# Kernel optimization log

Measured on AMD Instinct MI355X. Metric: run time of the kernel, lower is better.

Reference implementation:

```python
import jax, jax.numpy as jnp
import numpy as np

# Dims (match init_kwargs)
B, S, D = 2, 2048, 2048
H = 16
Q_LORA, KV_LORA = 768, 512
NOPE, ROPE, VD = 128, 64, 128
QHD = NOPE + ROPE  # 192


def setup_inputs() -> dict:
    key = jax.random.key(0)
    ks = jax.random.split(key, 7)
    w = lambda k, shape: (jax.random.normal(k, shape, jnp.float32) * 0.02)
    return {
        "x": jax.random.normal(ks[0], (B, S, D), jnp.float32),
        "position": jnp.broadcast_to(jnp.arange(S, dtype=jnp.int32), (B, S)),
        "mask": jnp.tril(jnp.ones((1, 1, S, S), jnp.int32)),  # causal
        "w_q_down": w(ks[1], (D, Q_LORA)),                 # (in, out) layout
        "w_q_up": w(ks[2], (Q_LORA, H * QHD)),
        "w_kv_down": w(ks[3], (D, KV_LORA + ROPE)),
        "w_kv_up": w(ks[4], (KV_LORA, H * (NOPE + VD))),
        "w_out": w(ks[5], (H * VD, D)),
    }


def reference(x, position, mask, w_q_down, w_q_up, w_kv_down, w_kv_up, w_out):
    # position unused: rope_embedding is None in the source module.
    # Low-rank Q: down then up projection.
    q = (x @ w_q_down) @ w_q_up                      # [B,S,H*QHD]
    q = q.reshape(B, S, H, QHD).transpose(0, 2, 1, 3)  # [B,H,S,QHD]
    q_nope, q_rope = q[..., :NOPE], q[..., NOPE:]

    # Low-rank KV: down projection yields compressed kv + shared rope key.
    c = x @ w_kv_down                                # [B,S,KV_LORA+ROPE]
    c_kv, k_rope = c[..., :KV_LORA], c[..., KV_LORA:]
    k_rope = k_rope[:, None, :, :]                   # [B,1,S,ROPE]

    kv = (c_kv @ w_kv_up).reshape(B, S, H, NOPE + VD).transpose(0, 2, 1, 3)
    k_nope, v = kv[..., :NOPE], kv[..., NOPE:]       # [B,H,S,NOPE], [B,H,S,VD]

    q_state = jnp.concatenate([q_nope, q_rope], axis=-1)           # [B,H,S,QHD]
    k_state = jnp.concatenate(
        [k_nope, jnp.broadcast_to(k_rope, (B, H, S, ROPE))], axis=-1)

    scale = 1.0 / jnp.sqrt(jnp.float32(VD))  # source divides by sqrt(v_head_dim)
    scores = jnp.einsum("bhqd,bhkd->bhqk", q_state, k_state) * scale
    scores = jnp.where(mask == 0, jnp.float32(-jnp.inf), scores)
    att = jax.nn.softmax(scores, axis=-1)            # dropout_rate=0 (eval)
    out = jnp.einsum("bhqk,bhkd->bhqd", att, v)      # [B,H,S,VD]
    out = out.transpose(0, 2, 1, 3).reshape(B, S, H * VD)
    return out @ w_out
```

## Files before the change

kernel.cpp:

```cpp
#include <hip/hip_runtime.h>

typedef __bf16 bf16;
typedef bf16 bf16x8 __attribute__((ext_vector_type(8)));
typedef bf16 bf16x4 __attribute__((ext_vector_type(4)));
typedef float f32x4 __attribute__((ext_vector_type(4)));
typedef short s16x4 __attribute__((ext_vector_type(4)));

#define AS1 __attribute__((address_space(1)))
#define AS3 __attribute__((address_space(3)))

__device__ __forceinline__ void load_lds16(const void* g, void* l) {
    __builtin_amdgcn_global_load_lds((const AS1 unsigned int*)g,
                                     (AS3 unsigned int*)l, 16, 0, 0);
}

__global__ __launch_bounds__(256) void cast_f32_bf16(
        const float* __restrict__ in, bf16* __restrict__ out, int n) {
    int i = (blockIdx.x * 256 + threadIdx.x) * 4;
    if (i < n) {
        float4 v = *(const float4*)(in + i);
        bf16x4 o = { (bf16)v.x, (bf16)v.y, (bf16)v.z, (bf16)v.w };
        *(bf16x4*)(out + i) = o;
    }
}

__global__ __launch_bounds__(256) void transpose_cast(
        const float* __restrict__ in, bf16* __restrict__ out,
        int K, int N, int Np) {
    __shared__ float tile[32][33];
    int bx = blockIdx.x * 32;
    int by = blockIdx.y * 32;
    int tx = threadIdx.x, ty = threadIdx.y;
#pragma unroll
    for (int i = 0; i < 4; ++i) {
        int k = by + ty + i * 8, n = bx + tx;
        float v = (k < K && n < N) ? in[(size_t)k * N + n] : 0.f;
        tile[ty + i * 8][tx] = v;
    }
    __syncthreads();
#pragma unroll
    for (int i = 0; i < 4; ++i) {
        int n = bx + ty + i * 8, k = by + tx;
        if (n < Np && k < K) out[(size_t)n * K + k] = (bf16)tile[tx][ty + i * 8];
    }
}

__global__ __launch_bounds__(256) void transpose_v(
        const bf16* __restrict__ kvb, bf16* __restrict__ vtb) {
    __shared__ bf16 t[32][34];
    const int kv0 = blockIdx.x * 32;
    const int vd0 = blockIdx.y * 32;
    const int bh = blockIdx.z;
    const int b = bh >> 4, h = bh & 15;
    const int tx = threadIdx.x, ty = threadIdx.y;
#pragma unroll
    for (int i = 0; i < 4; ++i)
        t[ty + i * 8][tx] = kvb[(size_t)(b * 2048 + kv0 + ty + i * 8) * 4096
                                + h * 256 + 128 + vd0 + tx];
    __syncthreads();
#pragma unroll
    for (int i = 0; i < 4; ++i)
        vtb[(size_t)(bh * 128 + vd0 + ty + i * 8) * 2048 + kv0 + tx] =
            t[tx][ty + i * 8];
}

template <typename OutT>
__global__ __launch_bounds__(256) void gemm_bt(
        const bf16* __restrict__ A, const bf16* __restrict__ Bt,
        OutT* __restrict__ C, int K, int lda, int ldb, int ldc) {
    __shared__ __align__(16) bf16 As[128 * 64];
    __shared__ __align__(16) bf16 Bs[128 * 64];
    const int tid = threadIdx.x;
    const int wave = tid >> 6, lane = tid & 63;
    const int l15 = lane & 15, quad = lane >> 4;
    const int m0 = blockIdx.y * 128, n0 = blockIdx.x * 128;
    const int wm = (wave >> 1) * 64, wn = (wave & 1) * 64;

    f32x4 acc[4][4] = {};

    for (int k0 = 0; k0 < K; k0 += 64) {
#pragma unroll
        for (int c = 0; c < 4; ++c) {
            int e = wave * 2048 + c * 512 + lane * 8;
            int r = e >> 6, col = e & 63;
            load_lds16(A + (size_t)(m0 + r) * lda + k0 + col,
                       &As[wave * 2048 + c * 512]);
            load_lds16(Bt + (size_t)(n0 + r) * ldb + k0 + col,
                       &Bs[wave * 2048 + c * 512]);
        }
        __syncthreads();
#pragma unroll
        for (int kk = 0; kk < 64; kk += 32) {
            bf16x8 af[4], bf[4];
#pragma unroll
            for (int i = 0; i < 4; ++i)
                af[i] = *(const bf16x8*)&As[(wm + i * 16 + l15) * 64 + kk + quad * 8];
#pragma unroll
            for (int j = 0; j < 4; ++j)
                bf[j] = *(const bf16x8*)&Bs[(wn + j * 16 + l15) * 64 + kk + quad * 8];
#pragma unroll
            for (int i = 0; i < 4; ++i)
#pragma unroll
                for (int j = 0; j < 4; ++j)
                    acc[i][j] = __builtin_amdgcn_mfma_f32_16x16x32_bf16(
                        af[i], bf[j], acc[i][j], 0, 0, 0);
        }
        __syncthreads();
    }
#pragma unroll
    for (int i = 0; i < 4; ++i)
#pragma unroll
        for (int j = 0; j < 4; ++j) {
            int row = m0 + wm + i * 16 + quad * 4;
            int col = n0 + wn + j * 16 + l15;
#pragma unroll
            for (int r = 0; r < 4; ++r)
                C[(size_t)(row + r) * ldc + col] = (OutT)acc[i][j][r];
        }
}

__global__ __launch_bounds__(256) void gemm_down(
        const bf16* __restrict__ A, const bf16* __restrict__ Bt,
        bf16* __restrict__ C1, bf16* __restrict__ C2) {
    const int K = 2048, lda = 2048, ldb = 2048;
    __shared__ __align__(16) bf16 As[128 * 64];
    __shared__ __align__(16) bf16 Bs[128 * 64];
    const int tid = threadIdx.x;
    const int wave = tid >> 6, lane = tid & 63;
    const int l15 = lane & 15, quad = lane >> 4;
    const int m0 = blockIdx.y * 128, n0 = blockIdx.x * 128;
    const int wm = (wave >> 1) * 64, wn = (wave & 1) * 64;

    f32x4 acc[4][4] = {};

    for (int k0 = 0; k0 < K; k0 += 64) {
#pragma unroll
        for (int c = 0; c < 4; ++c) {
            int e = wave * 2048 + c * 512 + lane * 8;
            int r = e >> 6, col = e & 63;
            load_lds16(A + (size_t)(m0 + r) * lda + k0 + col,
                       &As[wave * 2048 + c * 512]);
            load_lds16(Bt + (size_t)(n0 + r) * ldb + k0 + col,
                       &Bs[wave * 2048 + c * 512]);
        }
        __syncthreads();
#pragma unroll
        for (int kk = 0; kk < 64; kk += 32) {
            bf16x8 af[4], bf[4];
#pragma unroll
            for (int i = 0; i < 4; ++i)
                af[i] = *(const bf16x8*)&As[(wm + i * 16 + l15) * 64 + kk + quad * 8];
#pragma unroll
            for (int j = 0; j < 4; ++j)
                bf[j] = *(const bf16x8*)&Bs[(wn + j * 16 + l15) * 64 + kk + quad * 8];
#pragma unroll
            for (int i = 0; i < 4; ++i)
#pragma unroll
                for (int j = 0; j < 4; ++j)
                    acc[i][j] = __builtin_amdgcn_mfma_f32_16x16x32_bf16(
                        af[i], bf[j], acc[i][j], 0, 0, 0);
        }
        __syncthreads();
    }
    bf16* Cp; int ldc, coff;
    if (n0 < 768) { Cp = C1; ldc = 768; coff = 0; }
    else          { Cp = C2; ldc = 640; coff = 768; }
#pragma unroll
    for (int i = 0; i < 4; ++i)
#pragma unroll
        for (int j = 0; j < 4; ++j) {
            int row = m0 + wm + i * 16 + quad * 4;
            int col = n0 + wn + j * 16 + l15 - coff;
#pragma unroll
            for (int r = 0; r < 4; ++r)
                Cp[(size_t)(row + r) * ldc + col] = (bf16)acc[i][j][r];
        }
}

__global__ __launch_bounds__(1024, 4) void mla_attention_split(
        const bf16* __restrict__ qb, const bf16* __restrict__ kvb,
        const bf16* __restrict__ cb, const bf16* __restrict__ vtb,
        bf16* __restrict__ ob, bf16* __restrict__ part_o,
        float* __restrict__ part_ml) {
    constexpr int S = 2048;
    const signed char k_of[20]  = {7,7,7,7, 6,6,6,6, 5,5,5, 4,4,4, 3,3, 2,2, 1, 0};
    const signed char c_of[20]  = {0,1,2,3, 0,1,2,3, 0,1,2, 0,1,2, 0,1, 0,1, 0, 0};
    const signed char np_of[8]  = {1,1,2,2,3,3,4,4};
    const signed char pre_of[8] = {0,0,0,1,2,4,6,9};

    const int k  = k_of[blockIdx.x], c = c_of[blockIdx.x];
    const int np = np_of[k];
    const int h = blockIdx.y, b = blockIdx.z;
    const int T  = 4 * k + 4;
    const int t0 = (c * T) / np, t1 = ((c + 1) * T) / np;
    const int q0 = k * 256;

    const int tid = threadIdx.x, wave = tid >> 6, lane = tid & 63;
    const int l15 = lane & 15, quad = lane >> 4;

    __shared__ __align__(16) bf16 Ks[2][24 * 512];
    __shared__ __align__(16) bf16 Vs[2][8 * 1024];

    const int qrow = q0 + wave * 16 + l15;
    bf16x8 qf[6];
    {
        const bf16* qr = qb + (size_t)(b * S + qrow) * 3072 + h * 192;
#pragma unroll
        for (int ks = 0; ks < 6; ++ks)
            qf[ks] = *(const bf16x8*)(qr + ks * 32 + quad * 8);
    }

    const bf16* vt_head = vtb + (size_t)((b * 16 + h) * 128) * 2048;

    auto stage = [&](int kt, int bufi) {
        const int kv0 = kt * 64;
        if (wave < 8) {
            const int mt = wave >> 1;
            const size_t row = (size_t)(b * S + kv0 + mt * 16 + l15);
#pragma unroll
            for (int i = 0; i < 3; ++i) {
                const int ks = (wave & 1) * 3 + i;
                const bf16* g = (ks < 4)
                    ? kvb + row * 4096 + h * 256 + ks * 32 + quad * 8
                    : cb  + row * 640  + 512 + (ks - 4) * 32 + quad * 8;
                load_lds16(g, &Ks[bufi][(mt * 6 + ks) * 512]);
            }
        } else {
            const int nt = wave - 8;
#pragma unroll
            for (int i = 0; i < 2; ++i) {
                const bf16* g = vt_head + (size_t)(nt * 16 + l15) * 2048
                                + kv0 + (i * 4 + quad) * 8;
                load_lds16(g, &Vs[bufi][nt * 1024 + i * 512]);
            }
        }
    };

    f32x4 o[8] = {};
    float m_i = -1e30f, l_i = 0.f;
    const float sm_scale = 0.08838834764831845f * 1.4426950408889634f;
    const int qmin_w = q0 + wave * 16;

    stage(t0, 0);
    stage(t0 + 1, 1);

    int cur = 0;
    for (int kt = t0; kt < t1; ++kt, cur ^= 1) {
        const int kv0 = kt * 64;

        if (kt + 1 < t1) {
            if (wave < 8) asm volatile("s_waitcnt vmcnt(3)" ::: "memory");
            else          asm volatile("s_waitcnt vmcnt(2)" ::: "memory");
        } else {
            asm volatile("s_waitcnt vmcnt(0)" ::: "memory");
        }
        __builtin_amdgcn_s_barrier();
        __builtin_amdgcn_sched_barrier(0);

        f32x4 s[4];
        __builtin_amdgcn_s_setprio(1);
#pragma unroll
        for (int mt = 0; mt < 4; ++mt) {
            f32x4 a = {};
#pragma unroll
            for (int ks = 0; ks < 6; ++ks) {
                bf16x8 kf = *(const bf16x8*)&Ks[cur][(mt * 6 + ks) * 512 + lane * 8];
                a = __builtin_amdgcn_mfma_f32_16x16x32_bf16(kf, qf[ks], a, 0, 0, 0);
            }
            s[mt] = a;
        }
        __builtin_amdgcn_s_setprio(0);

        if (kv0 + 63 > qmin_w) {
#pragma unroll
            for (int mt = 0; mt < 4; ++mt)
#pragma unroll
                for (int r = 0; r < 4; ++r) {
                    int kvi = kv0 + mt * 16 + quad * 4 + r;
                    s[mt][r] = (kvi <= qrow) ? s[mt][r] * sm_scale : -1e30f;
                }
        } else {
#pragma unroll
            for (int mt = 0; mt < 4; ++mt)
#pragma unroll
                for (int r = 0; r < 4; ++r)
                    s[mt][r] = s[mt][r] * sm_scale;
        }
        float mx4[4];
#pragma unroll
        for (int mt = 0; mt < 4; ++mt)
            mx4[mt] = fmaxf(fmaxf(s[mt][0], s[mt][1]),
                            fmaxf(s[mt][2], s[mt][3]));
        float mx = fmaxf(fmaxf(mx4[0], mx4[1]), fmaxf(mx4[2], mx4[3]));
        mx = fmaxf(mx, __shfl_xor(mx, 16, 64));
        mx = fmaxf(mx, __shfl_xor(mx, 32, 64));
        float m_new = fmaxf(m_i, mx);
        float su4[4];
        bf16x4 pf[4];
#pragma unroll
        for (int mt = 0; mt < 4; ++mt) {
            float e0 = exp2f(s[mt][0] - m_new);
            float e1 = exp2f(s[mt][1] - m_new);
            float e2 = exp2f(s[mt][2] - m_new);
            float e3 = exp2f(s[mt][3] - m_new);
            su4[mt] = (e0 + e1) + (e2 + e3);
            pf[mt][0] = (bf16)e0; pf[mt][1] = (bf16)e1;
            pf[mt][2] = (bf16)e2; pf[mt][3] = (bf16)e3;
        }
        float su = (su4[0] + su4[1]) + (su4[2] + su4[3]);
        su += __shfl_xor(su, 16, 64);
        su += __shfl_xor(su, 32, 64);
        if (__all(mx <= m_i)) {
            l_i += su;
        } else {
            float alpha = exp2f(m_i - m_new);
            l_i = l_i * alpha + su;
            m_i = m_new;
            float alpha_r[4];
#pragma unroll
            for (int r = 0; r < 4; ++r)
                alpha_r[r] = __shfl(alpha, quad * 4 + r, 64);
#pragma unroll
            for (int nt = 0; nt < 8; ++nt)
#pragma unroll
                for (int r = 0; r < 4; ++r) o[nt][r] *= alpha_r[r];
        }

        __builtin_amdgcn_s_setprio(1);
#pragma unroll
        for (int ktk = 0; ktk < 4; ++ktk) {
            s16x4 a = __builtin_bit_cast(s16x4, pf[ktk]);
            const int voff = ktk * 256 + (quad >> 1) * 128 + l15 * 8 + (quad & 1) * 4;
#pragma unroll
            for (int nt = 0; nt < 8; ++nt) {
                s16x4 bfv = __builtin_bit_cast(s16x4,
                    *(const bf16x4*)&Vs[cur][nt * 1024 + voff]);
                o[nt] = __builtin_amdgcn_mfma_f32_16x16x16bf16_1k(a, bfv, o[nt], 0, 0, 0);
            }
        }
        __builtin_amdgcn_s_setprio(0);

        __builtin_amdgcn_s_barrier();
        if (kt + 2 < t1) stage(kt + 2, cur);
    }

    if (np == 1) {
        float l_r[4];
#pragma unroll
        for (int r = 0; r < 4; ++r) l_r[r] = __shfl(l_i, quad * 4 + r, 64);
        bf16* obase = ob + (size_t)(b * S + q0 + wave * 16) * 2048 + h * 128;
#pragma unroll
        for (int nt = 0; nt < 8; ++nt)
#pragma unroll
            for (int r = 0; r < 4; ++r)
                obase[(size_t)(quad * 4 + r) * 2048 + nt * 16 + l15] =
                    (bf16)(o[nt][r] / l_r[r]);
    } else {
        const int bh = b * 16 + h;
        if (quad == 0) {
            const int qlocal = wave * 16 + l15;
            float* mlp = part_ml + ((size_t)(bh * 8 + k) * 4 + c) * 512;
            mlp[qlocal] = m_i;
            mlp[256 + qlocal] = l_i;
        }
        if (c == np - 1) {
            bf16* obase = ob + (size_t)(b * S + q0 + wave * 16) * 2048 + h * 128;
#pragma unroll
            for (int nt = 0; nt < 8; ++nt)
#pragma unroll
                for (int r = 0; r < 4; ++r)
                    obase[(size_t)(quad * 4 + r) * 2048 + nt * 16 + l15] =
                        (bf16)o[nt][r];
        } else {
            bf16* pb = part_o + (size_t)(bh * 12 + pre_of[k] + c) * 32768
                       + (size_t)(wave * 16) * 128;
#pragma unroll
            for (int nt = 0; nt < 8; ++nt)
#pragma unroll
                for (int r = 0; r < 4; ++r)
                    pb[(quad * 4 + r) * 128 + nt * 16 + l15] = (bf16)o[nt][r];
        }
    }
}

__global__ __launch_bounds__(256) void mla_merge(
        const bf16* __restrict__ part_o, const float* __restrict__ part_ml,
        bf16* __restrict__ ob) {
    const signed char np_of[8]  = {1,1,2,2,3,3,4,4};
    const signed char pre_of[8] = {0,0,0,1,2,4,6,9};
    const int k = 2 + blockIdx.x;
    const int h = blockIdx.y, b = blockIdx.z;
    const int bh = b * 16 + h;
    const int np = np_of[k];
    const int row = threadIdx.x;

    const float* mlb = part_ml + (size_t)(bh * 8 + k) * 4 * 512;
    const float m0 = mlb[row],            l0 = mlb[256 + row];
    const float m1 = mlb[512 + row],      l1 = mlb[512 + 256 + row];
    const float m2 = (np > 2) ? mlb[1024 + row] : -1e30f;
    const float l2 = (np > 2) ? mlb[1024 + 256 + row] : 0.f;
    const float m3 = (np > 3) ? mlb[1536 + row] : -1e30f;
    const float l3 = (np > 3) ? mlb[1536 + 256 + row] : 0.f;
    const float M = fmaxf(fmaxf(m0, m1), fmaxf(m2, m3));
    float a0 = exp2f(m0 - M), a1 = exp2f(m1 - M);
    float a2 = exp2f(m2 - M), a3 = exp2f(m3 - M);
    const float inv = 1.f / (l0 * a0 + l1 * a1 + l2 * a2 + l3 * a3);
    a0 *= inv; a1 *= inv; a2 *= inv; a3 *= inv;
    const float alast = (np == 2) ? a1 : (np == 3) ? a2 : a3;

    const bf16* p0 = part_o + (size_t)(bh * 12 + pre_of[k]) * 32768 + row * 128;
    const bf16* p1 = p0 + 32768;
    const bf16* p2 = p1 + 32768;
    bf16* po = ob + (size_t)(b * 2048 + k * 256 + row) * 2048 + h * 128;
#pragma unroll
    for (int i = 0; i < 16; ++i) {
        bf16x8 vb = *(const bf16x8*)(po + i * 8);
        bf16x8 v0 = *(const bf16x8*)(p0 + i * 8);
        float acc[8];
#pragma unroll
        for (int u = 0; u < 8; ++u)
            acc[u] = (float)vb[u] * alast + (float)v0[u] * a0;
        if (np > 2) {
            bf16x8 v1 = *(const bf16x8*)(p1 + i * 8);
#pragma unroll
            for (int u = 0; u < 8; ++u) acc[u] += (float)v1[u] * a1;
        }
        if (np > 3) {
            bf16x8 v2 = *(const bf16x8*)(p2 + i * 8);
#pragma unroll
            for (int u = 0; u < 8; ++u) acc[u] += (float)v2[u] * a2;
        }
        bf16x8 om;
#pragma unroll
        for (int u = 0; u < 8; ++u) om[u] = (bf16)acc[u];
        *(bf16x8*)(po + i * 8) = om;
    }
}

extern "C" void kernel_launch(void* const* d_in, const int* in_sizes, int n_in,
                              void* d_out, int out_size, void* d_ws, size_t ws_size,
                              hipStream_t stream) {
    const float* x    = (const float*)d_in[0];
    const float* wqd  = (const float*)d_in[3];
    const float* wqu  = (const float*)d_in[4];
    const float* wkvd = (const float*)d_in[5];
    const float* wkvu = (const float*)d_in[6];
    const float* wout = (const float*)d_in[7];
    float* out = (float*)d_out;
    char* ws = (char*)d_ws;

    bf16* xb    = (bf16*)(ws + 0);
    bf16* vtb   = (bf16*)(ws + 0);
    bf16* wqdT  = (bf16*)(ws + 16777216);
    bf16* wkvdT = (bf16*)(ws + 19922944);
    bf16* wquT  = (bf16*)(ws + 22544384);
    bf16* wkvuT = (bf16*)(ws + 27262976);
    float* part_ml = (float*)(ws + 16777216);
    bf16* part_o  = (bf16*)out;
    bf16* woutT = (bf16*)(ws + 31457280);
    bf16* qd    = (bf16*)(ws + 39845888);
    bf16* qb    = (bf16*)(ws + 46137344);
    bf16* cb    = (bf16*)(ws + 71303168);
    bf16* kvb   = (bf16*)(ws + 76546048);
    bf16* attnb = (bf16*)(ws + 110100480);

    dim3 tb(32, 8);
    cast_f32_bf16<<<8192, 256, 0, stream>>>(x, xb, 8388608);
    transpose_cast<<<dim3(24, 64),  tb, 0, stream>>>(wqd,  wqdT,  2048, 768,  768);
    transpose_cast<<<dim3(20, 64),  tb, 0, stream>>>(wkvd, wkvdT, 2048, 576,  640);
    transpose_cast<<<dim3(96, 24),  tb, 0, stream>>>(wqu,  wquT,  768,  3072, 3072);
    transpose_cast<<<dim3(128, 16), tb, 0, stream>>>(wkvu, wkvuT, 512,  4096, 4096);
    transpose_cast<<<dim3(64, 64),  tb, 0, stream>>>(wout, woutT, 2048, 2048, 2048);

    gemm_down<<<dim3(11, 32), 256, 0, stream>>>(xb, wqdT, qd, cb);
    gemm_bt<bf16><<<dim3(24, 32), 256, 0, stream>>>(qd, wquT,  qb,  768, 768, 768, 3072);
    gemm_bt<bf16><<<dim3(32, 32), 256, 0, stream>>>(cb, wkvuT, kvb, 512, 640, 512, 4096);

    transpose_v<<<dim3(64, 4, 32), tb, 0, stream>>>(kvb, vtb);

    mla_attention_split<<<dim3(20, 16, 2), 1024, 0, stream>>>(
        qb, kvb, cb, vtb, attnb, part_o, part_ml);
    mla_merge<<<dim3(6, 16, 2), 256, 0, stream>>>(part_o, part_ml, attnb);

    gemm_bt<float><<<dim3(16, 32), 256, 0, stream>>>(attnb, woutT, out, 2048, 2048, 2048, 2048);
}
```

Measured before the change: 480.2 us.

## Single-buffer V tile in attention, prefetching V one tile ahead

Splits the K and V staging so K stays double-buffered two tiles ahead, while V uses a single LDS buffer loaded one tile ahead and waited on just before the PV matmul. This halves V's LDS footprint, which may allow more resident blocks per CU. In exchange it adds an extra barrier per iteration and leaves less time to hide V load latency.

```diff
diff --git a/kernel.cpp b/kernel.cpp
--- a/kernel.cpp
+++ b/kernel.cpp
@@ -199,7 +199,7 @@
     const int l15 = lane & 15, quad = lane >> 4;
 
     __shared__ __align__(16) bf16 Ks[2][24 * 512];
-    __shared__ __align__(16) bf16 Vs[2][8 * 1024];
+    __shared__ __align__(16) bf16 Vs[8 * 1024];
 
     const int qrow = q0 + wave * 16 + l15;
     bf16x8 qf[6];
@@ -212,9 +212,9 @@
 
     const bf16* vt_head = vtb + (size_t)((b * 16 + h) * 128) * 2048;
 
-    auto stage = [&](int kt, int bufi) {
-        const int kv0 = kt * 64;
+    auto stage_k = [&](int kt, int bufi) {
         if (wave < 8) {
+            const int kv0 = kt * 64;
             const int mt = wave >> 1;
             const size_t row = (size_t)(b * S + kv0 + mt * 16 + l15);
 #pragma unroll
@@ -225,13 +225,17 @@
                     : cb  + row * 640  + 512 + (ks - 4) * 32 + quad * 8;
                 load_lds16(g, &Ks[bufi][(mt * 6 + ks) * 512]);
             }
-        } else {
+        }
+    };
+    auto stage_v = [&](int kt) {
+        if (wave >= 8) {
+            const int kv0 = kt * 64;
             const int nt = wave - 8;
 #pragma unroll
             for (int i = 0; i < 2; ++i) {
                 const bf16* g = vt_head + (size_t)(nt * 16 + l15) * 2048
                                 + kv0 + (i * 4 + quad) * 8;
-                load_lds16(g, &Vs[bufi][nt * 1024 + i * 512]);
+                load_lds16(g, &Vs[nt * 1024 + i * 512]);
             }
         }
     };
@@ -241,18 +245,17 @@
     const float sm_scale = 0.08838834764831845f * 1.4426950408889634f;
     const int qmin_w = q0 + wave * 16;
 
-    stage(t0, 0);
-    stage(t0 + 1, 1);
+    stage_k(t0, 0);
+    stage_v(t0);
+    stage_k(t0 + 1, 1);
 
     int cur = 0;
     for (int kt = t0; kt < t1; ++kt, cur ^= 1) {
         const int kv0 = kt * 64;
 
-        if (kt + 1 < t1) {
-            if (wave < 8) asm volatile("s_waitcnt vmcnt(3)" ::: "memory");
-            else          asm volatile("s_waitcnt vmcnt(2)" ::: "memory");
-        } else {
-            asm volatile("s_waitcnt vmcnt(0)" ::: "memory");
+        if (wave < 8) {
+            if (kt + 1 < t1) asm volatile("s_waitcnt vmcnt(3)" ::: "memory");
+            else             asm volatile("s_waitcnt vmcnt(0)" ::: "memory");
         }
         __builtin_amdgcn_s_barrier();
         __builtin_amdgcn_sched_barrier(0);
@@ -326,6 +329,10 @@
                 for (int r = 0; r < 4; ++r) o[nt][r] *= alpha_r[r];
         }
 
+        if (wave >= 8) asm volatile("s_waitcnt vmcnt(0)" ::: "memory");
+        __builtin_amdgcn_s_barrier();
+        __builtin_amdgcn_sched_barrier(0);
+
         __builtin_amdgcn_s_setprio(1);
 #pragma unroll
         for (int ktk = 0; ktk < 4; ++ktk) {
@@ -334,14 +341,15 @@
 #pragma unroll
             for (int nt = 0; nt < 8; ++nt) {
                 s16x4 bfv = __builtin_bit_cast(s16x4,
-                    *(const bf16x4*)&Vs[cur][nt * 1024 + voff]);
+                    *(const bf16x4*)&Vs[nt * 1024 + voff]);
                 o[nt] = __builtin_amdgcn_mfma_f32_16x16x16bf16_1k(a, bfv, o[nt], 0, 0, 0);
             }
         }
         __builtin_amdgcn_s_setprio(0);
 
         __builtin_amdgcn_s_barrier();
-        if (kt + 2 < t1) stage(kt + 2, cur);
+        if (kt + 2 < t1) stage_k(kt + 2, cur);
+        if (kt + 1 < t1) stage_v(kt + 1);
     }
 
     if (np == 1) {
```

Measured after the change: 495.5 us. +3.2%, slower.
